# Performance work log

Hardware: AMD Instinct MI355X
Metric: run time of the kernel (lower is better)

The kernel has to match this reference:

```python
import jax, jax.numpy as jnp
import numpy as np

N, CX, CS, H = 2048, 768, 384, 16
D = CX // H  # 48


def _ln(t, eps=1e-5):
    mu = jnp.mean(t, axis=-1, keepdims=True)
    var = jnp.mean(jnp.square(t - mu), axis=-1, keepdims=True)
    return (t - mu) * jax.lax.rsqrt(var + eps)


def setup_inputs() -> dict:
    key = jax.random.key(0)
    ks = jax.random.split(key, 16)
    s = 0.02
    return {
        "x": jax.random.normal(ks[0], (N, CX), jnp.float32),
        "mask": jax.random.randint(ks[1], (N,), 0, 2, jnp.int32),
        "pair_logits": jax.random.normal(ks[2], (H, N, N), jnp.float32),
        "single_cond": jax.random.normal(ks[3], (N, CS), jnp.float32),
        # AdaptiveLayerNorm params (single_cond LN has weight, no bias)
        "ln_sc_w": jnp.ones((CS,), jnp.float32),
        "sc_scale_w": s * jax.random.normal(ks[4], (CS, CX), jnp.float32),
        "sc_scale_b": jnp.zeros((CX,), jnp.float32),
        "sc_bias_w": s * jax.random.normal(ks[5], (CS, CX), jnp.float32),
        # q/k/v/gating projections (stored as (in, out); y = x @ W)
        "q_w": s * jax.random.normal(ks[6], (CX, CX), jnp.float32),
        "q_b": jnp.zeros((CX,), jnp.float32),
        "k_w": s * jax.random.normal(ks[7], (CX, CX), jnp.float32),
        "v_w": s * jax.random.normal(ks[8], (CX, CX), jnp.float32),
        "gate_w": s * jax.random.normal(ks[9], (CX, CX), jnp.float32),
        # AdaLNZero params
        "out_w": s * jax.random.normal(ks[10], (CX, CX), jnp.float32),
        "azc_w": s * jax.random.normal(ks[11], (CS, CX), jnp.float32),
        "azc_b": jnp.zeros((CX,), jnp.float32),
    }


def reference(x, mask, pair_logits, single_cond, ln_sc_w, sc_scale_w, sc_scale_b,
              sc_bias_w, q_w, q_b, k_w, v_w, gate_w, out_w, azc_w, azc_b):
    # AdaptiveLayerNorm (use_single_cond=True)
    xn = _ln(x)                              # (N, CX), no affine
    sc = _ln(single_cond) * ln_sc_w          # (N, CS), weight only
    xa = jax.nn.sigmoid(sc @ sc_scale_w + sc_scale_b) * xn + sc @ sc_bias_w

    # QKV projections, split into heads: (N, H, D)
    q = (xa @ q_w + q_b).reshape(N, H, D)
    k = (xa @ k_w).reshape(N, H, D)
    v = (xa @ v_w).reshape(N, H, D)

    # Attention with per-head additive pair bias and key mask
    logits = jnp.einsum("qhd,khd->hqk", q * (D ** -0.5), k) + pair_logits
    logits = jnp.where(mask.astype(bool)[None, None, :], logits, -1e9)
    w = jax.nn.softmax(logits, axis=-1)      # (H, N, N)
    wa = jnp.einsum("hqk,khd->qhd", w, v).reshape(N, CX)

    # Gating, then AdaLNZero output
    wa = wa * jax.nn.sigmoid(xa @ gate_w)
    out = (wa @ out_w) * jax.nn.sigmoid(sc @ azc_w + azc_b)
    return out
```

## Files before the change

kernel.cpp:

```cpp
#include <hip/hip_runtime.h>
#include <math.h>

#define NN 2048
#define CXX 768
#define CSS 384
#define HH 16
#define DHH 48
#define KSPLIT 2

typedef short bf16x8 __attribute__((ext_vector_type(8)));
typedef float f32x4 __attribute__((ext_vector_type(4)));

#define MFMA16(a,b,c) __builtin_amdgcn_mfma_f32_16x16x32_bf16(a,b,c,0,0,0)

__device__ __forceinline__ unsigned short f2bf(float f){
  unsigned u = __float_as_uint(f);
  u += 0x7FFFu + ((u >> 16) & 1u);
  return (unsigned short)(u >> 16);
}
__device__ __forceinline__ float bf2f(unsigned short u){
  return __uint_as_float(((unsigned)u) << 16);
}
__device__ __forceinline__ void async_copy16(const void* g, void* l){
  __builtin_amdgcn_global_load_lds((const __attribute__((address_space(1))) void*)g,
                                   (__attribute__((address_space(3))) void*)l, 16, 0, 0);
}

__device__ inline float waveReduceSum(float v){
  #pragma unroll
  for(int o=32;o>0;o>>=1) v += __shfl_xor(v,o);
  return v;
}

__global__ __launch_bounds__(256) void transpose_all(
    const float* __restrict__ s0, const float* __restrict__ s1, const float* __restrict__ s2,
    const float* __restrict__ s3, const float* __restrict__ s4, const float* __restrict__ s5,
    const float* __restrict__ s6, const float* __restrict__ s7,
    unsigned short* __restrict__ d_scale, unsigned short* __restrict__ d_bias,
    unsigned short* __restrict__ d_azc, unsigned short* __restrict__ d_qkvg,
    unsigned short* __restrict__ d_out){
  int z = blockIdx.z;
  const float* W; unsigned short* Wt; int K;
  switch(z){
    case 0: W=s0; Wt=d_scale; K=384; break;
    case 1: W=s1; Wt=d_bias;  K=384; break;
    case 2: W=s2; Wt=d_azc;   K=384; break;
    case 3: W=s3; Wt=d_qkvg + 0*589824; K=768; break;
    case 4: W=s4; Wt=d_qkvg + 1*589824; K=768; break;
    case 5: W=s5; Wt=d_qkvg + 2*589824; K=768; break;
    case 6: W=s6; Wt=d_qkvg + 3*589824; K=768; break;
    default: W=s7; Wt=d_out; K=768; break;
  }
  int n0 = blockIdx.x*32, k0 = blockIdx.y*32;
  if(k0 >= K) return;
  __shared__ unsigned short t[32][33];
  int c = threadIdx.x & 31, r = threadIdx.x >> 5;
  #pragma unroll
  for(int i=0;i<32;i+=8){
    float v = W[(size_t)(k0 + r + i)*CXX + n0 + c];
    t[c][r+i] = f2bf(v);
  }
  __syncthreads();
  #pragma unroll
  for(int i=0;i<32;i+=8){
    Wt[(size_t)(n0 + r + i)*K + k0 + c] = t[r+i][c];
  }
}

__global__ __launch_bounds__(384) void ln_fused(const float* __restrict__ x,
    const float* __restrict__ scin, const float* __restrict__ w,
    float* __restrict__ xn, unsigned short* __restrict__ scb){
  int row = blockIdx.x;
  int t = threadIdx.x;
  int wid = t>>6, lane = t&63;
  __shared__ float red[6];
  float a0 = x[(size_t)row*CXX + t];
  float a1 = x[(size_t)row*CXX + 384 + t];
  float s = waveReduceSum(a0+a1);
  if(lane==0) red[wid]=s;
  __syncthreads();
  float mu = (red[0]+red[1]+red[2]+red[3]+red[4]+red[5]) * (1.0f/CXX);
  float d0=a0-mu, d1=a1-mu;
  float q = waveReduceSum(d0*d0+d1*d1);
  __syncthreads();
  if(lane==0) red[wid]=q;
  __syncthreads();
  float var = (red[0]+red[1]+red[2]+red[3]+red[4]+red[5]) * (1.0f/CXX);
  float r = rsqrtf(var + 1e-5f);
  xn[(size_t)row*CXX + t] = d0*r;
  xn[(size_t)row*CXX + 384 + t] = d1*r;
  float b = scin[(size_t)row*CSS + t];
  float s2 = waveReduceSum(b);
  __syncthreads();
  if(lane==0) red[wid]=s2;
  __syncthreads();
  float mu2 = (red[0]+red[1]+red[2]+red[3]+red[4]+red[5]) * (1.0f/CSS);
  float d2 = b - mu2;
  float q2 = waveReduceSum(d2*d2);
  __syncthreads();
  if(lane==0) red[wid]=q2;
  __syncthreads();
  float var2 = (red[0]+red[1]+red[2]+red[3]+red[4]+red[5]) * (1.0f/CSS);
  float r2 = rsqrtf(var2 + 1e-5f);
  scb[(size_t)row*CSS + t] = f2bf(d2*r2*w[t]);
}

__global__ __launch_bounds__(256) void gemm_qkvg(const unsigned short* __restrict__ A,
    const unsigned short* __restrict__ Bt, const float* __restrict__ bias,
    unsigned short* __restrict__ C, unsigned short* __restrict__ vt){
  __shared__ unsigned short As[128*32];
  __shared__ unsigned short Bs[128*32];
  const int tid = threadIdx.x;
  const int w = tid>>6, lane = tid&63;
  const int ln15 = lane&15, hi = lane>>4;
  const int wm = w&1, wn = w>>1;
  const int m0 = blockIdx.y*128, n0 = blockIdx.x*128;
  const int lrow = lane>>2, lk = (lane&3)*8;
  const int K = 768, NC = 3072;

  f32x4 z = {0.f,0.f,0.f,0.f};
  f32x4 acc[4][4];
  #pragma unroll
  for(int i=0;i<4;i++)
    #pragma unroll
    for(int j=0;j<4;j++) acc[i][j] = z;

  for(int k0=0;k0<K;k0+=32){
    const unsigned short* ga = A + (size_t)(m0 + w*32 + lrow)*K + k0 + lk;
    const unsigned short* gb = Bt + (size_t)(n0 + w*32 + lrow)*K + k0 + lk;
    async_copy16(ga,          &As[w*1024]);
    async_copy16(ga + 16*K,   &As[w*1024 + 512]);
    async_copy16(gb,          &Bs[w*1024]);
    async_copy16(gb + 16*K,   &Bs[w*1024 + 512]);
    __syncthreads();
    bf16x8 af[4], bfr[4];
    #pragma unroll
    for(int i=0;i<4;i++) af[i]  = *(const bf16x8*)&As[(wm*64 + i*16 + ln15)*32 + hi*8];
    #pragma unroll
    for(int j=0;j<4;j++) bfr[j] = *(const bf16x8*)&Bs[(wn*64 + j*16 + ln15)*32 + hi*8];
    #pragma unroll
    for(int i=0;i<4;i++)
      #pragma unroll
      for(int j=0;j<4;j++)
        acc[i][j] = MFMA16(af[i], bfr[j], acc[i][j]);
    __syncthreads();
  }

  #pragma unroll
  for(int i=0;i<4;i++)
    #pragma unroll
    for(int j=0;j<4;j++){
      int gm0 = m0 + wm*64 + i*16 + hi*4;
      int gn  = n0 + wn*64 + j*16 + ln15;
      if(gn >= 1536 && gn < 2304){
        ushort4 v4;
        v4.x = f2bf(acc[i][j][0]);
        v4.y = f2bf(acc[i][j][1]);
        v4.z = f2bf(acc[i][j][2]);
        v4.w = f2bf(acc[i][j][3]);
        *(ushort4*)&vt[(size_t)(gn - 1536)*NN + gm0] = v4;
      } else {
        #pragma unroll
        for(int r=0;r<4;r++){
          float v = acc[i][j][r];
          if(gn < 768) v += bias[gn];
          if(gn >= 2304) v = 1.0f/(1.0f + __expf(-v));
          C[(size_t)(gm0+r)*NC + gn] = f2bf(v);
        }
      }
    }
}

__global__ __launch_bounds__(256) void adaln3(const unsigned short* __restrict__ A,
    const unsigned short* __restrict__ B1, const unsigned short* __restrict__ B2,
    const unsigned short* __restrict__ B3, const float* __restrict__ bs,
    const float* __restrict__ zb, const float* __restrict__ xn,
    unsigned short* __restrict__ xa, float* __restrict__ azc){
  __shared__ unsigned short As[64*32];
  __shared__ unsigned short Bs1[64*32];
  __shared__ unsigned short Bs2[64*32];
  __shared__ unsigned short Bs3[64*32];
  const int tid = threadIdx.x;
  const int w = tid>>6, lane = tid&63;
  const int ln15 = lane&15, hi = lane>>4;
  const int wm = w&1, wn = w>>1;
  const int m0 = blockIdx.y*64, n0 = blockIdx.x*64;
  const int lrow = tid>>2, lk = (tid&3)*8;
  const int K = CSS;

  f32x4 z = {0.f,0.f,0.f,0.f};
  f32x4 acc1[2][2], acc2[2][2], acc3[2][2];
  #pragma unroll
  for(int i=0;i<2;i++)
    #pragma unroll
    for(int j=0;j<2;j++){ acc1[i][j]=z; acc2[i][j]=z; acc3[i][j]=z; }

  for(int k0=0;k0<K;k0+=32){
    async_copy16(A  + (size_t)(m0+lrow)*K + k0 + lk, &As [w*512]);
    async_copy16(B1 + (size_t)(n0+lrow)*K + k0 + lk, &Bs1[w*512]);
    async_copy16(B2 + (size_t)(n0+lrow)*K + k0 + lk, &Bs2[w*512]);
    async_copy16(B3 + (size_t)(n0+lrow)*K + k0 + lk, &Bs3[w*512]);
    __syncthreads();
    bf16x8 af[2], b1f[2], b2f[2], b3f[2];
    #pragma unroll
    for(int i=0;i<2;i++) af[i]  = *(const bf16x8*)&As[(wm*32 + i*16 + ln15)*32 + hi*8];
    #pragma unroll
    for(int j=0;j<2;j++){
      b1f[j] = *(const bf16x8*)&Bs1[(wn*32 + j*16 + ln15)*32 + hi*8];
      b2f[j] = *(const bf16x8*)&Bs2[(wn*32 + j*16 + ln15)*32 + hi*8];
      b3f[j] = *(const bf16x8*)&Bs3[(wn*32 + j*16 + ln15)*32 + hi*8];
    }
    #pragma unroll
    for(int i=0;i<2;i++)
      #pragma unroll
      for(int j=0;j<2;j++){
        acc1[i][j] = MFMA16(af[i], b1f[j], acc1[i][j]);
        acc2[i][j] = MFMA16(af[i], b2f[j], acc2[i][j]);
        acc3[i][j] = MFMA16(af[i], b3f[j], acc3[i][j]);
      }
    __syncthreads();
  }

  #pragma unroll
  for(int i=0;i<2;i++)
    #pragma unroll
    for(int j=0;j<2;j++)
      #pragma unroll
      for(int r=0;r<4;r++){
        int gm = m0 + wm*32 + i*16 + hi*4 + r;
        int gn = n0 + wn*32 + j*16 + ln15;
        float g = 1.0f/(1.0f + __expf(-(acc1[i][j][r] + bs[gn])));
        float v = g * xn[(size_t)gm*CXX + gn] + acc2[i][j][r];
        xa[(size_t)gm*CXX + gn] = f2bf(v);
        azc[(size_t)gm*CXX + gn] = 1.0f/(1.0f + __expf(-(acc3[i][j][r] + zb[gn])));
      }
}

__global__ __launch_bounds__(256) void gemm_out(const unsigned short* __restrict__ A,
    const unsigned short* __restrict__ Bt, const float* __restrict__ mul,
    float* __restrict__ C){
  __shared__ unsigned short As[64*32];
  __shared__ unsigned short Bs[64*32];
  const int tid = threadIdx.x;
  const int w = tid>>6, lane = tid&63;
  const int ln15 = lane&15, hi = lane>>4;
  const int wm = w&1, wn = w>>1;
  const int m0 = blockIdx.y*64, n0 = blockIdx.x*64;
  const int lrow = tid>>2, lk = (tid&3)*8;
  const int K = 768;

  f32x4 z = {0.f,0.f,0.f,0.f};
  f32x4 acc[2][2];
  #pragma unroll
  for(int i=0;i<2;i++)
    #pragma unroll
    for(int j=0;j<2;j++) acc[i][j]=z;

  for(int k0=0;k0<K;k0+=32){
    async_copy16(A  + (size_t)(m0+lrow)*K + k0 + lk, &As[w*512]);
    async_copy16(Bt + (size_t)(n0+lrow)*K + k0 + lk, &Bs[w*512]);
    __syncthreads();
    bf16x8 af[2], bfr[2];
    #pragma unroll
    for(int i=0;i<2;i++) af[i]  = *(const bf16x8*)&As[(wm*32 + i*16 + ln15)*32 + hi*8];
    #pragma unroll
    for(int j=0;j<2;j++) bfr[j] = *(const bf16x8*)&Bs[(wn*32 + j*16 + ln15)*32 + hi*8];
    #pragma unroll
    for(int i=0;i<2;i++)
      #pragma unroll
      for(int j=0;j<2;j++)
        acc[i][j] = MFMA16(af[i], bfr[j], acc[i][j]);
    __syncthreads();
  }

  #pragma unroll
  for(int i=0;i<2;i++)
    #pragma unroll
    for(int j=0;j<2;j++)
      #pragma unroll
      for(int r=0;r<4;r++){
        int gm = m0 + wm*32 + i*16 + hi*4 + r;
        int gn = n0 + wn*32 + j*16 + ln15;
        C[(size_t)gm*CXX + gn] = acc[i][j][r] * mul[(size_t)gm*CXX + gn];
      }
}


#define LOAD_TILE(B, KOFF) do{                                                     \
    int kk_ = (KOFF);                                                              \
    _Pragma("unroll")                                                              \
    for(int jt=0;jt<4;jt++){                                                       \
      const unsigned short* kp_ = qkvg + (size_t)(kk_ + jt*16 + ln15)*3072 + 768 + h*DHH + hi*8; \
      kf0[B][jt] = *(const bf16x8*)kp_;                                            \
      kf1[B][jt] = *(const bf16x8*)(kp_ + 32);                                     \
    }                                                                              \
    _Pragma("unroll")                                                              \
    for(int jt=0;jt<4;jt++) mkr[B][jt] = mask[kk_ + jt*16 + ln15];                 \
    const float* pb_ = pair + ((size_t)h*NN + (size_t)(q0+qrb))*NN + kk_ + ln15;   \
    _Pragma("unroll")                                                              \
    for(int r=0;r<4;r++)                                                           \
      _Pragma("unroll")                                                            \
      for(int jt=0;jt<4;jt++)                                                      \
        pfr[B][jt][r] = pb_[(size_t)r*NN + jt*16];                                 \
  }while(0)

#define ATTN_TILE(B, NB, KCUR, KNXT) do{                                           \
    bf16x8 vf0[3], vf1[3];                                                         \
    _Pragma("unroll")                                                              \
    for(int dt=0;dt<3;dt++){                                                       \
      const unsigned short* vp_ = vt + (size_t)(h*DHH + dt*16 + ln15)*NN + (KCUR) + hi*8; \
      vf0[dt] = *(const bf16x8*)vp_;                                               \
      vf1[dt] = *(const bf16x8*)(vp_ + 32);                                        \
    }                                                                              \
    f32x4 sreg[4];                                                                 \
    __builtin_amdgcn_s_setprio(1);                                                 \
    _Pragma("unroll")                                                              \
    for(int jt=0;jt<4;jt++){                                                       \
      f32x4 s_ = z;                                                                \
      s_ = MFMA16(aq0, kf0[B][jt], s_);                                            \
      s_ = MFMA16(aq1, kf1[B][jt], s_);                                            \
      sreg[jt] = s_;                                                               \
    }                                                                              \
    __builtin_amdgcn_s_setprio(0);                                                 \
    LOAD_TILE(NB, KNXT);                                                           \
    float sv[4][4];                                                                \
    _Pragma("unroll")                                                              \
    for(int jt=0;jt<4;jt++)                                                        \
      _Pragma("unroll")                                                            \
      for(int r=0;r<4;r++)                                                         \
        sv[jt][r] = mkr[B][jt] ? sreg[jt][r]*scale + pfr[B][jt][r] : -1e9f;        \
    float mrow[4], al[4], rs[4];                                                   \
    _Pragma("unroll")                                                              \
    for(int r=0;r<4;r++)                                                           \
      mrow[r] = fmaxf(fmaxf(sv[0][r],sv[1][r]), fmaxf(sv[2][r],sv[3][r]));         \
    _Pragma("unroll")                                                              \
    for(int o=1;o<16;o<<=1)                                                        \
      _Pragma("unroll")                                                            \
      for(int r=0;r<4;r++) mrow[r] = fmaxf(mrow[r], __shfl_xor(mrow[r],o));        \
    _Pragma("unroll")                                                              \
    for(int r=0;r<4;r++){                                                          \
      float mn_ = fmaxf(mold[r], mrow[r]);                                         \
      al[r] = __expf(mold[r] - mn_);                                               \
      mold[r] = mn_;                                                               \
    }                                                                              \
    float pv[4][4];                                                                \
    _Pragma("unroll")                                                              \
    for(int jt=0;jt<4;jt++)                                                        \
      _Pragma("unroll")                                                            \
      for(int r=0;r<4;r++)                                                         \
        pv[jt][r] = __expf(sv[jt][r] - mold[r]);                                   \
    _Pragma("unroll")                                                              \
    for(int r=0;r<4;r++) rs[r] = pv[0][r]+pv[1][r]+pv[2][r]+pv[3][r];              \
    _Pragma("unroll")                                                              \
    for(int o=1;o<16;o<<=1)                                                        \
      _Pragma("unroll")                                                            \
      for(int r=0;r<4;r++) rs[r] += __shfl_xor(rs[r],o);                           \
    _Pragma("unroll")                                                              \
    for(int r=0;r<4;r++) l[r] = l[r]*al[r] + rs[r];                                \
    _Pragma("unroll")                                                              \
    for(int jt=0;jt<4;jt++)                                                        \
      _Pragma("unroll")                                                            \
      for(int r=0;r<4;r++)                                                         \
        Ps[w][(hi*4+r)*72 + jt*16 + ln15] = f2bf(pv[jt][r]);                       \
    __asm__ volatile("s_waitcnt lgkmcnt(0)" ::: "memory");                         \
    _Pragma("unroll")                                                              \
    for(int dt=0;dt<3;dt++)                                                        \
      _Pragma("unroll")                                                            \
      for(int r=0;r<4;r++) oacc[dt][r] *= al[r];                                   \
    bf16x8 ap0 = *(const bf16x8*)&Ps[w][ln15*72 + hi*8];                           \
    bf16x8 ap1 = *(const bf16x8*)&Ps[w][ln15*72 + 32 + hi*8];                      \
    __builtin_amdgcn_s_setprio(1);                                                 \
    _Pragma("unroll")                                                              \
    for(int dt=0;dt<3;dt++){                                                       \
      oacc[dt] = MFMA16(ap0, vf0[dt], oacc[dt]);                                   \
      oacc[dt] = MFMA16(ap1, vf1[dt], oacc[dt]);                                   \
    }                                                                              \
    __builtin_amdgcn_s_setprio(0);                                                 \
  }while(0)

__global__ __launch_bounds__(256) void attn_mfma(const unsigned short* __restrict__ qkvg,
    const unsigned short* __restrict__ vt, const float* __restrict__ pair,
    const int* __restrict__ mask, float* __restrict__ po, float* __restrict__ pm,
    float* __restrict__ pl){
  const int h = blockIdx.y;
  const int q0 = blockIdx.x*64;
  const int kz = blockIdx.z;
  const int kbase = kz*(NN/KSPLIT);
  const int NT = (NN/KSPLIT)/64;
  const int tid = threadIdx.x;
  const int w = tid>>6, lane = tid&63;
  const int ln15 = lane&15, hi = lane>>4;
  const int qrb = w*16 + hi*4;

  __shared__ unsigned short Ps[4][16*72];

  const float scale = 0.14433756729740643f;
  f32x4 z = {0.f,0.f,0.f,0.f};

  const unsigned short* qp = qkvg + (size_t)(q0 + w*16 + ln15)*3072 + h*DHH + hi*8;
  bf16x8 aq0 = *(const bf16x8*)qp;
  bf16x8 aq1 = *(const bf16x8*)(qp + 32);
  {
    bf16x8 z8 = {0,0,0,0,0,0,0,0};
    if(hi >= 2) aq1 = z8;
  }

  f32x4 oacc[3] = {z,z,z};
  float mold[4] = {-1e30f,-1e30f,-1e30f,-1e30f};
  float l[4] = {0.f,0.f,0.f,0.f};

  bf16x8 kf0[2][4], kf1[2][4];
  float  pfr[2][4][4];
  int    mkr[2][4];

  LOAD_TILE(0, kbase);

  for(int t=0; t<NT/2; ++t){
    int k0c = kbase + (2*t)*64;
    int k1c = kbase + (2*t+1)*64;
    int k2n = (2*t+2 < NT) ? kbase + (2*t+2)*64 : kbase;
    ATTN_TILE(0, 1, k0c, k1c);
    ATTN_TILE(1, 0, k1c, k2n);
  }

  #pragma unroll
  for(int r=0;r<4;r++){
    int qrow = q0 + qrb + r;
    size_t rowi = (size_t)(kz*HH + h)*NN + qrow;
    #pragma unroll
    for(int dt=0;dt<3;dt++)
      po[rowi*DHH + dt*16 + ln15] = oacc[dt][r];
    if(ln15==0){
      pm[rowi] = mold[r];
      pl[rowi] = l[r];
    }
  }
}

__global__ __launch_bounds__(256) void attn_combine(const float* __restrict__ po,
    const float* __restrict__ pm, const float* __restrict__ pl,
    const unsigned short* __restrict__ qkvg, unsigned short* __restrict__ wag){
  const int row = blockIdx.x*4 + (threadIdx.x>>6);
  const int lane = threadIdx.x & 63;
  #pragma unroll
  for(int i=0;i<12;i++){
    int c = lane + i*64;
    int hh = c / DHH, d = c - hh*DHH;
    size_t r0 = (size_t)hh*NN + row;
    size_t r1 = (size_t)(HH + hh)*NN + row;
    float m0 = pm[r0], m1 = pm[r1];
    float M = fmaxf(m0, m1);
    float e0 = __expf(m0 - M), e1 = __expf(m1 - M);
    float L = pl[r0]*e0 + pl[r1]*e1;
    float v = (po[r0*DHH + d]*e0 + po[r1*DHH + d]*e1) / L;
    float g = bf2f(qkvg[(size_t)row*3072 + 2304 + c]);
    wag[(size_t)row*CXX + c] = f2bf(v * g);
  }
}

extern "C" void kernel_launch(void* const* d_in, const int* in_sizes, int n_in,
                              void* d_out, int out_size, void* d_ws, size_t ws_size,
                              hipStream_t stream) {
  const float* x           = (const float*)d_in[0];
  const int*   mask        = (const int*)  d_in[1];
  const float* pair        = (const float*)d_in[2];
  const float* single_cond = (const float*)d_in[3];
  const float* ln_sc_w     = (const float*)d_in[4];
  const float* sc_scale_w  = (const float*)d_in[5];
  const float* sc_scale_b  = (const float*)d_in[6];
  const float* sc_bias_w   = (const float*)d_in[7];
  const float* q_w         = (const float*)d_in[8];
  const float* q_b         = (const float*)d_in[9];
  const float* k_w         = (const float*)d_in[10];
  const float* v_w         = (const float*)d_in[11];
  const float* gate_w      = (const float*)d_in[12];
  const float* out_w       = (const float*)d_in[13];
  const float* azc_w       = (const float*)d_in[14];
  const float* azc_b       = (const float*)d_in[15];
  float* out = (float*)d_out;

  unsigned short* p = (unsigned short*)d_ws;
  unsigned short* Wt_scale = p;  p += 768*384;
  unsigned short* Wt_bias  = p;  p += 768*384;
  unsigned short* Wt_azc   = p;  p += 768*384;
  unsigned short* Wt_out   = p;  p += 768*768;
  unsigned short* Wt_qkvg  = p;  p += (size_t)3072*768;
  unsigned short* scb      = p;  p += 2048*384;
  unsigned short* xa       = p;  p += 2048*768;
  unsigned short* qkvg     = p;  p += (size_t)2048*3072;
  unsigned short* wag      = p;  p += 2048*768;
  unsigned short* vt       = p;  p += (size_t)768*2048;
  float* fp = (float*)p;
  float* xn  = fp; fp += (size_t)2048*768;
  float* azc = fp; fp += (size_t)2048*768;
  float* po  = fp; fp += (size_t)KSPLIT*HH*NN*DHH;
  float* pm  = fp; fp += (size_t)KSPLIT*HH*NN;
  float* pl  = fp;

  transpose_all<<<dim3(24,24,8), 256, 0, stream>>>(
      sc_scale_w, sc_bias_w, azc_w, q_w, k_w, v_w, gate_w, out_w,
      Wt_scale, Wt_bias, Wt_azc, Wt_qkvg, Wt_out);

  ln_fused<<<NN, 384, 0, stream>>>(x, single_cond, ln_sc_w, xn, scb);

  adaln3<<<dim3(12,32), 256, 0, stream>>>(scb, Wt_scale, Wt_bias, Wt_azc,
                                          sc_scale_b, azc_b, xn, xa, azc);

  gemm_qkvg<<<dim3(24,16), 256, 0, stream>>>(xa, Wt_qkvg, q_b, qkvg, vt);

  attn_mfma<<<dim3(32,16,KSPLIT), 256, 0, stream>>>(qkvg, vt, pair, mask, po, pm, pl);

  attn_combine<<<512, 256, 0, stream>>>(po, pm, pl, qkvg, wag);

  gemm_out<<<dim3(12,32), 256, 0, stream>>>(wag, Wt_out, azc, out);
}
```

Baseline: 539.3 us.

## Transpose attention MFMA layout so each lane owns one query row; split keys four ways

Swaps the MFMA operand order so S^T and O^T are computed, giving each lane a single query row. Row max and sum then need two cross-lane shuffles instead of four per register. Pair-bias and mask reads become float4/int4 loads along contiguous keys, and P is packed into LDS as 32-bit words. KSPLIT rises from 2 to 4 for more parallel blocks, and the combine kernel is generalized to merge any number of partial softmax splits, at the cost of more partial-output traffic.

```diff
diff --git a/kernel.cpp b/kernel.cpp
--- a/kernel.cpp
+++ b/kernel.cpp
@@ -6,7 +6,7 @@
 #define CSS 384
 #define HH 16
 #define DHH 48
-#define KSPLIT 2
+#define KSPLIT 4
 
 typedef short bf16x8 __attribute__((ext_vector_type(8)));
 typedef float f32x4 __attribute__((ext_vector_type(4)));
@@ -286,29 +286,14 @@
 }
 
 
-#define LOAD_TILE(B, KOFF) do{                                                     \
-    int kk_ = (KOFF);                                                              \
-    _Pragma("unroll")                                                              \
-    for(int jt=0;jt<4;jt++){                                                       \
-      const unsigned short* kp_ = qkvg + (size_t)(kk_ + jt*16 + ln15)*3072 + 768 + h*DHH + hi*8; \
-      kf0[B][jt] = *(const bf16x8*)kp_;                                            \
-      kf1[B][jt] = *(const bf16x8*)(kp_ + 32);                                     \
-    }                                                                              \
-    _Pragma("unroll")                                                              \
-    for(int jt=0;jt<4;jt++) mkr[B][jt] = mask[kk_ + jt*16 + ln15];                 \
-    const float* pb_ = pair + ((size_t)h*NN + (size_t)(q0+qrb))*NN + kk_ + ln15;   \
-    _Pragma("unroll")                                                              \
-    for(int r=0;r<4;r++)                                                           \
-      _Pragma("unroll")                                                            \
-      for(int jt=0;jt<4;jt++)                                                      \
-        pfr[B][jt][r] = pb_[(size_t)r*NN + jt*16];                                 \
-  }while(0)
-
-#define ATTN_TILE(B, NB, KCUR, KNXT) do{                                           \
+#define ATTN_STEP(KF0C, KF1C, PFC, KF0N, KF1N, KK, KNXT, KP2) do{                  \
+    int4 mk[4];                                                                    \
+    _Pragma("unroll")                                                              \
+    for(int jt=0;jt<4;jt++) mk[jt] = *(const int4*)&mask[(KK) + jt*16 + hi*4];     \
     bf16x8 vf0[3], vf1[3];                                                         \
     _Pragma("unroll")                                                              \
     for(int dt=0;dt<3;dt++){                                                       \
-      const unsigned short* vp_ = vt + (size_t)(h*DHH + dt*16 + ln15)*NN + (KCUR) + hi*8; \
+      const unsigned short* vp_ = vt + (size_t)(h*DHH + dt*16 + ln15)*NN + (KK) + hi*8; \
       vf0[dt] = *(const bf16x8*)vp_;                                               \
       vf1[dt] = *(const bf16x8*)(vp_ + 32);                                        \
     }                                                                              \
@@ -317,63 +302,69 @@
     _Pragma("unroll")                                                              \
     for(int jt=0;jt<4;jt++){                                                       \
       f32x4 s_ = z;                                                                \
-      s_ = MFMA16(aq0, kf0[B][jt], s_);                                            \
-      s_ = MFMA16(aq1, kf1[B][jt], s_);                                            \
+      s_ = MFMA16(KF0C[jt], bq0, s_);                                              \
+      s_ = MFMA16(KF1C[jt], bq1, s_);                                              \
       sreg[jt] = s_;                                                               \
     }                                                                              \
     __builtin_amdgcn_s_setprio(0);                                                 \
-    LOAD_TILE(NB, KNXT);                                                           \
+    _Pragma("unroll")                                                              \
+    for(int jt=0;jt<4;jt++){                                                       \
+      const unsigned short* kp_ = qkvg + (size_t)((KNXT) + jt*16 + ln15)*3072 + 768 + h*DHH + hi*8; \
+      KF0N[jt] = *(const bf16x8*)kp_;                                              \
+      KF1N[jt] = *(const bf16x8*)(kp_ + 32);                                       \
+    }                                                                              \
     float sv[4][4];                                                                \
+    _Pragma("unroll")                                                              \
+    for(int jt=0;jt<4;jt++){                                                       \
+      sv[jt][0] = mk[jt].x ? sreg[jt][0]*scale + PFC[jt].x : -1e9f;                \
+      sv[jt][1] = mk[jt].y ? sreg[jt][1]*scale + PFC[jt].y : -1e9f;                \
+      sv[jt][2] = mk[jt].z ? sreg[jt][2]*scale + PFC[jt].z : -1e9f;                \
+      sv[jt][3] = mk[jt].w ? sreg[jt][3]*scale + PFC[jt].w : -1e9f;                \
+    }                                                                              \
+    _Pragma("unroll")                                                              \
+    for(int jt=0;jt<4;jt++)                                                        \
+      PFC[jt] = *(const float4*)&pbase[(KP2) + jt*16 + hi*4];                      \
+    float vmax = sv[0][0];                                                         \
     _Pragma("unroll")                                                              \
     for(int jt=0;jt<4;jt++)                                                        \
       _Pragma("unroll")                                                            \
-      for(int r=0;r<4;r++)                                                         \
-        sv[jt][r] = mkr[B][jt] ? sreg[jt][r]*scale + pfr[B][jt][r] : -1e9f;        \
-    float mrow[4], al[4], rs[4];                                                   \
-    _Pragma("unroll")                                                              \
-    for(int r=0;r<4;r++)                                                           \
-      mrow[r] = fmaxf(fmaxf(sv[0][r],sv[1][r]), fmaxf(sv[2][r],sv[3][r]));         \
-    _Pragma("unroll")                                                              \
-    for(int o=1;o<16;o<<=1)                                                        \
-      _Pragma("unroll")                                                            \
-      for(int r=0;r<4;r++) mrow[r] = fmaxf(mrow[r], __shfl_xor(mrow[r],o));        \
-    _Pragma("unroll")                                                              \
-    for(int r=0;r<4;r++){                                                          \
-      float mn_ = fmaxf(mold[r], mrow[r]);                                         \
-      al[r] = __expf(mold[r] - mn_);                                               \
-      mold[r] = mn_;                                                               \
-    }                                                                              \
+      for(int r=0;r<4;r++) vmax = fmaxf(vmax, sv[jt][r]);                          \
+    vmax = fmaxf(vmax, __shfl_xor(vmax,16));                                       \
+    vmax = fmaxf(vmax, __shfl_xor(vmax,32));                                       \
+    float mn = fmaxf(m_run, vmax);                                                 \
+    float al = __expf(m_run - mn);                                                 \
+    m_run = mn;                                                                    \
     float pv[4][4];                                                                \
+    float rs = 0.f;                                                                \
     _Pragma("unroll")                                                              \
     for(int jt=0;jt<4;jt++)                                                        \
       _Pragma("unroll")                                                            \
-      for(int r=0;r<4;r++)                                                         \
-        pv[jt][r] = __expf(sv[jt][r] - mold[r]);                                   \
-    _Pragma("unroll")                                                              \
-    for(int r=0;r<4;r++) rs[r] = pv[0][r]+pv[1][r]+pv[2][r]+pv[3][r];              \
-    _Pragma("unroll")                                                              \
-    for(int o=1;o<16;o<<=1)                                                        \
-      _Pragma("unroll")                                                            \
-      for(int r=0;r<4;r++) rs[r] += __shfl_xor(rs[r],o);                           \
-    _Pragma("unroll")                                                              \
-    for(int r=0;r<4;r++) l[r] = l[r]*al[r] + rs[r];                                \
-    _Pragma("unroll")                                                              \
-    for(int jt=0;jt<4;jt++)                                                        \
-      _Pragma("unroll")                                                            \
-      for(int r=0;r<4;r++)                                                         \
-        Ps[w][(hi*4+r)*72 + jt*16 + ln15] = f2bf(pv[jt][r]);                       \
+      for(int r=0;r<4;r++){                                                        \
+        pv[jt][r] = __expf(sv[jt][r] - mn);                                        \
+        rs += pv[jt][r];                                                           \
+      }                                                                            \
+    rs += __shfl_xor(rs,16);                                                       \
+    rs += __shfl_xor(rs,32);                                                       \
+    l_run = l_run*al + rs;                                                         \
+    _Pragma("unroll")                                                              \
+    for(int jt=0;jt<4;jt++){                                                       \
+      unsigned int w0_ = (unsigned)f2bf(pv[jt][0]) | ((unsigned)f2bf(pv[jt][1])<<16); \
+      unsigned int w1_ = (unsigned)f2bf(pv[jt][2]) | ((unsigned)f2bf(pv[jt][3])<<16); \
+      *(uint2*)&Pme[ln15*36 + jt*8 + hi*2] = make_uint2(w0_,w1_);                  \
+    }                                                                              \
     __asm__ volatile("s_waitcnt lgkmcnt(0)" ::: "memory");                         \
+    __builtin_amdgcn_sched_barrier(0);                                             \
     _Pragma("unroll")                                                              \
     for(int dt=0;dt<3;dt++)                                                        \
       _Pragma("unroll")                                                            \
-      for(int r=0;r<4;r++) oacc[dt][r] *= al[r];                                   \
-    bf16x8 ap0 = *(const bf16x8*)&Ps[w][ln15*72 + hi*8];                           \
-    bf16x8 ap1 = *(const bf16x8*)&Ps[w][ln15*72 + 32 + hi*8];                      \
+      for(int r=0;r<4;r++) oacc[dt][r] *= al;                                      \
+    bf16x8 bp0 = *(const bf16x8*)&Pme[ln15*36 + hi*4];                             \
+    bf16x8 bp1 = *(const bf16x8*)&Pme[ln15*36 + 16 + hi*4];                        \
     __builtin_amdgcn_s_setprio(1);                                                 \
     _Pragma("unroll")                                                              \
     for(int dt=0;dt<3;dt++){                                                       \
-      oacc[dt] = MFMA16(ap0, vf0[dt], oacc[dt]);                                   \
-      oacc[dt] = MFMA16(ap1, vf1[dt], oacc[dt]);                                   \
+      oacc[dt] = MFMA16(vf0[dt], bp0, oacc[dt]);                                   \
+      oacc[dt] = MFMA16(vf1[dt], bp1, oacc[dt]);                                   \
     }                                                                              \
     __builtin_amdgcn_s_setprio(0);                                                 \
   }while(0)
@@ -390,51 +381,53 @@
   const int tid = threadIdx.x;
   const int w = tid>>6, lane = tid&63;
   const int ln15 = lane&15, hi = lane>>4;
-  const int qrb = w*16 + hi*4;
-
-  __shared__ unsigned short Ps[4][16*72];
+  const int q = q0 + w*16 + ln15;
+
+  __shared__ unsigned int Pw[4][16*36];
+  unsigned int* Pme = &Pw[w][0];
 
   const float scale = 0.14433756729740643f;
   f32x4 z = {0.f,0.f,0.f,0.f};
 
-  const unsigned short* qp = qkvg + (size_t)(q0 + w*16 + ln15)*3072 + h*DHH + hi*8;
-  bf16x8 aq0 = *(const bf16x8*)qp;
-  bf16x8 aq1 = *(const bf16x8*)(qp + 32);
-  {
-    bf16x8 z8 = {0,0,0,0,0,0,0,0};
-    if(hi >= 2) aq1 = z8;
-  }
+  const unsigned short* qp = qkvg + (size_t)q*3072 + h*DHH + hi*8;
+  bf16x8 bq0 = *(const bf16x8*)qp;
+  bf16x8 bq1 = *(const bf16x8*)(qp + 32);
+  if(hi >= 2){ bf16x8 z8 = {0,0,0,0,0,0,0,0}; bq1 = z8; }
 
   f32x4 oacc[3] = {z,z,z};
-  float mold[4] = {-1e30f,-1e30f,-1e30f,-1e30f};
-  float l[4] = {0.f,0.f,0.f,0.f};
-
-  bf16x8 kf0[2][4], kf1[2][4];
-  float  pfr[2][4][4];
-  int    mkr[2][4];
-
-  LOAD_TILE(0, kbase);
-
-  for(int t=0; t<NT/2; ++t){
-    int k0c = kbase + (2*t)*64;
-    int k1c = kbase + (2*t+1)*64;
-    int k2n = (2*t+2 < NT) ? kbase + (2*t+2)*64 : kbase;
-    ATTN_TILE(0, 1, k0c, k1c);
-    ATTN_TILE(1, 0, k1c, k2n);
-  }
-
-  #pragma unroll
-  for(int r=0;r<4;r++){
-    int qrow = q0 + qrb + r;
-    size_t rowi = (size_t)(kz*HH + h)*NN + qrow;
-    #pragma unroll
-    for(int dt=0;dt<3;dt++)
-      po[rowi*DHH + dt*16 + ln15] = oacc[dt][r];
-    if(ln15==0){
-      pm[rowi] = mold[r];
-      pl[rowi] = l[r];
-    }
-  }
+  float m_run = -1e30f, l_run = 0.f;
+
+  bf16x8 kf0a[4], kf1a[4], kf0b[4], kf1b[4];
+  float4 pfa[4], pfb[4];
+
+  const float* pbase = pair + ((size_t)h*NN + q)*NN;
+
+  #pragma unroll
+  for(int jt=0;jt<4;jt++){
+    const unsigned short* kp = qkvg + (size_t)(kbase + jt*16 + ln15)*3072 + 768 + h*DHH + hi*8;
+    kf0a[jt] = *(const bf16x8*)kp;
+    kf1a[jt] = *(const bf16x8*)(kp+32);
+    pfa[jt] = *(const float4*)&pbase[kbase + jt*16 + hi*4];
+    pfb[jt] = *(const float4*)&pbase[kbase + 64 + jt*16 + hi*4];
+  }
+
+  for(int t=0; t<NT; t+=2){
+    const int kk = kbase + t*64;
+    const int kp2a = (t+2 < NT) ? kk + 128 : kbase;
+    const int kp2b = (t+3 < NT) ? kk + 192 : kbase;
+    const int knb  = (t+2 < NT) ? kk + 128 : kbase;
+    ATTN_STEP(kf0a, kf1a, pfa, kf0b, kf1b, kk,      kk+64, kp2a);
+    ATTN_STEP(kf0b, kf1b, pfb, kf0a, kf1a, kk+64,   knb,   kp2b);
+  }
+
+  size_t rowi = ((size_t)(kz*HH + h))*NN + q;
+  #pragma unroll
+  for(int dt=0;dt<3;dt++){
+    float4 o4;
+    o4.x = oacc[dt][0]; o4.y = oacc[dt][1]; o4.z = oacc[dt][2]; o4.w = oacc[dt][3];
+    *(float4*)&po[rowi*DHH + dt*16 + hi*4] = o4;
+  }
+  if(hi==0){ pm[rowi] = m_run; pl[rowi] = l_run; }
 }
 
 __global__ __launch_bounds__(256) void attn_combine(const float* __restrict__ po,
@@ -446,15 +439,23 @@
   for(int i=0;i<12;i++){
     int c = lane + i*64;
     int hh = c / DHH, d = c - hh*DHH;
-    size_t r0 = (size_t)hh*NN + row;
-    size_t r1 = (size_t)(HH + hh)*NN + row;
-    float m0 = pm[r0], m1 = pm[r1];
-    float M = fmaxf(m0, m1);
-    float e0 = __expf(m0 - M), e1 = __expf(m1 - M);
-    float L = pl[r0]*e0 + pl[r1]*e1;
-    float v = (po[r0*DHH + d]*e0 + po[r1*DHH + d]*e1) / L;
+    float mv[KSPLIT];
+    float M = -1e30f;
+    #pragma unroll
+    for(int s=0;s<KSPLIT;s++){
+      mv[s] = pm[((size_t)(s*HH + hh))*NN + row];
+      M = fmaxf(M, mv[s]);
+    }
+    float L = 0.f, V = 0.f;
+    #pragma unroll
+    for(int s=0;s<KSPLIT;s++){
+      size_t rr = ((size_t)(s*HH + hh))*NN + row;
+      float e = __expf(mv[s] - M);
+      L += pl[rr]*e;
+      V += po[rr*DHH + d]*e;
+    }
     float g = bf2f(qkvg[(size_t)row*3072 + 2304 + c]);
-    wag[(size_t)row*CXX + c] = f2bf(v * g);
+    wag[(size_t)row*CXX + c] = f2bf((V/L) * g);
   }
 }
 
```

Measured after the change: 566.3 us. 5.0% more time.
